# Kernel tuning notes

Measured on AMD Instinct MI355X. Metric: run time of the kernel, lower is better.

## Reference

```python
import jax, jax.numpy as jnp
import numpy as np

T, B, I, H = 512, 32, 512, 512

def setup_inputs() -> dict:
    key = jax.random.key(0)
    k1, k2, k3 = jax.random.split(key, 3)
    x = jax.random.normal(k1, (T, B, I), dtype=jnp.float32)
    h0 = jnp.zeros((B, H), dtype=jnp.float32)
    W_ih = jax.random.normal(k2, (3 * H, I), dtype=jnp.float32) * (1.0 / np.sqrt(H))
    # diagonal recurrent weights, one vector per gate (r, z, n), uniform(-1, 1)
    w_hh = jax.random.uniform(k3, (3, H), dtype=jnp.float32, minval=-1.0, maxval=1.0)
    return {"x": x, "h0": h0, "W_ih": W_ih, "w_hh": w_hh}

def reference(x, h0, W_ih, w_hh):
    # Precompute input-side gate pre-activations for all timesteps: (T, B, 3H)
    gx = jnp.einsum('tbi,gi->tbg', x, W_ih)
    xr, xz, xn = jnp.split(gx, 3, axis=-1)  # each (T, B, H)
    w_r, w_z, w_n = w_hh[0], w_hh[1], w_hh[2]  # each (H,)

    def step(h, g):
        gr, gz, gn = g
        r = jax.nn.sigmoid(gr + w_r * h)
        z = jax.nn.sigmoid(gz + w_z * h)
        n = jnp.tanh(gn + r * (w_n * h))
        h_new = (1.0 - z) * n + z * h
        return h_new, h_new

    h_last, out = jax.lax.scan(step, h0, (xr, xz, xn))
    # out: (T, B, H) all hidden states; h_last: (1, B, H) final state (GRU convention)
    return out, h_last[None, :, :]
```

## Files before the change

kernel.cpp:

```cpp
#include <hip/hip_runtime.h>
#include <hip/hip_bf16.h>
#include <stdint.h>

#define T_DIM 512
#define B_DIM 32
#define K_DIM 512
#define H_DIM 512
#define N_DIM 1536
#define M_DIM 16384

typedef __bf16 bf16_t;
typedef bf16_t bf16x8 __attribute__((ext_vector_type(8)));
typedef float floatx4 __attribute__((ext_vector_type(4)));

#define LOG2E 1.442695041f
#define TWO_LOG2E 2.885390082f

__device__ __forceinline__ unsigned int f2bf_bits(float f) {
  uint32_t u = __builtin_bit_cast(uint32_t, f);
  u += 0x7FFFu + ((u >> 16) & 1u);
  return u >> 16;
}

__global__ void convert_both_kernel(const float* __restrict__ x,
                                    unsigned short* __restrict__ xb,
                                    const float* __restrict__ W,
                                    unsigned short* __restrict__ Wb) {
  int bid = blockIdx.x;
  const float* in;
  unsigned short* out;
  int i;
  if (bid < 4096) {
    in = x; out = xb; i = (bid * 256 + threadIdx.x) * 8;
  } else {
    in = W; out = Wb; i = ((bid - 4096) * 256 + threadIdx.x) * 8;
  }
  const float4* p = (const float4*)(in + i);
  float4 f0 = p[0];
  float4 f1 = p[1];
  uint4 v;
  v.x = f2bf_bits(f0.x) | (f2bf_bits(f0.y) << 16);
  v.y = f2bf_bits(f0.z) | (f2bf_bits(f0.w) << 16);
  v.z = f2bf_bits(f1.x) | (f2bf_bits(f1.y) << 16);
  v.w = f2bf_bits(f1.z) | (f2bf_bits(f1.w) << 16);
  *(uint4*)(out + i) = v;
}

__global__ __launch_bounds__(256) void gemm_bf16_kernel(
    const unsigned short* __restrict__ A, const unsigned short* __restrict__ Bm,
    float* __restrict__ C) {
  __shared__ bf16_t smem[16384];
  const int tid = threadIdx.x;
  const int lane = tid & 63;
  const int w = tid >> 6;
  const int tileM = blockIdx.x * 128;
  const int tileN = blockIdx.y * 128;
  const int waveM = w & 1;
  const int waveN = w >> 1;
  const int lm = lane & 15;
  const int lg = lane >> 4;

  floatx4 acc[4][4] = {};

  for (int k0 = 0; k0 < K_DIM; k0 += 64) {
#pragma unroll
    for (int j = 0; j < 4; ++j) {
      int s = j * 256 + tid;
      int row = s >> 3;
      int cpos = s & 7;
      int kc = cpos ^ (row & 7);
      bf16_t* la = smem + (j * 256 + w * 64) * 8;
      const unsigned short* ga = A + (size_t)(tileM + row) * K_DIM + k0 + kc * 8;
      __builtin_amdgcn_global_load_lds(
          (const __attribute__((address_space(1))) unsigned int*)ga,
          (__attribute__((address_space(3))) unsigned int*)la, 16, 0, 0);
      bf16_t* lb = smem + 8192 + (j * 256 + w * 64) * 8;
      const unsigned short* gb = Bm + (size_t)(tileN + row) * K_DIM + k0 + kc * 8;
      __builtin_amdgcn_global_load_lds(
          (const __attribute__((address_space(1))) unsigned int*)gb,
          (__attribute__((address_space(3))) unsigned int*)lb, 16, 0, 0);
    }
    __syncthreads();

#pragma unroll
    for (int ks = 0; ks < 2; ++ks) {
      bf16x8 af[4], bfg[4];
#pragma unroll
      for (int i = 0; i < 4; ++i) {
        int row = waveM * 64 + i * 16 + lm;
        int c = ks * 4 + lg;
        af[i] = *(const bf16x8*)(smem + row * 64 + (c ^ (row & 7)) * 8);
      }
#pragma unroll
      for (int j = 0; j < 4; ++j) {
        int row = waveN * 64 + j * 16 + lm;
        int c = ks * 4 + lg;
        bfg[j] = *(const bf16x8*)(smem + 8192 + row * 64 + (c ^ (row & 7)) * 8);
      }
#pragma unroll
      for (int i = 0; i < 4; ++i)
#pragma unroll
        for (int j = 0; j < 4; ++j)
          acc[i][j] = __builtin_amdgcn_mfma_f32_16x16x32_bf16(af[i], bfg[j],
                                                              acc[i][j], 0, 0, 0);
    }
    __syncthreads();
  }

  const int row0 = tileM + waveM * 64 + (lane >> 4) * 4;
  const int col0 = tileN + waveN * 64 + lm;
#pragma unroll
  for (int i = 0; i < 4; ++i)
#pragma unroll
    for (int j = 0; j < 4; ++j) {
      const int col = col0 + j * 16;
      const float scl = (col >= 2 * H_DIM) ? TWO_LOG2E : -LOG2E;
#pragma unroll
      for (int r = 0; r < 4; ++r)
        C[(size_t)(row0 + i * 16 + r) * N_DIM + col] = scl * acc[i][j][r];
    }
}

__global__ __launch_bounds__(64) void indgru_scan_kernel(
    const float* __restrict__ gx, const float* __restrict__ h0,
    const float* __restrict__ w_hh, float* __restrict__ out,
    float* __restrict__ hlast) {
  const int idx = blockIdx.x * 64 + threadIdx.x;
  const int b = idx >> 9;
  const int h = idx & (H_DIM - 1);
  const float wr = -LOG2E * w_hh[h];
  const float wz = -LOG2E * w_hh[H_DIM + h];
  const float wn = TWO_LOG2E * w_hh[2 * H_DIM + h];
  float hv = h0[idx];

  const float* base = gx + (size_t)b * N_DIM + H_DIM + h;
  float* outp = out + (size_t)b * H_DIM + h;

  constexpr int D = 16;
  float pr[D], pz[D], pn[D];
#pragma unroll
  for (int t = 0; t < D; ++t) {
    const float* p = base + (size_t)t * (B_DIM * N_DIM);
    pr[t] = p[-H_DIM];
    pz[t] = p[0];
    pn[t] = p[H_DIM];
  }

  for (int t0 = 0; t0 < T_DIM - D; t0 += D) {
#pragma unroll
    for (int s = 0; s < D; ++s) {
      const int t = t0 + s;
      float gr = pr[s], gz = pz[s], gn = pn[s];
      const float* p = base + (size_t)(t + D) * (B_DIM * N_DIM);
      pr[s] = p[-H_DIM];
      pz[s] = p[0];
      pn[s] = p[H_DIM];
      float ar = fmaf(wr, hv, gr);
      float az = fmaf(wz, hv, gz);
      float t1 = wn * hv;
      float er = __builtin_amdgcn_exp2f(ar);
      float ez = __builtin_amdgcn_exp2f(az);
      float r = __builtin_amdgcn_rcpf(1.0f + er);
      float z = __builtin_amdgcn_rcpf(1.0f + ez);
      float en = __builtin_amdgcn_exp2f(fmaf(r, t1, gn));
      float u = __builtin_amdgcn_rcpf(1.0f + en);
      float n = fmaf(-2.0f, u, 1.0f);
      float zh = z * hv;
      float omz = 1.0f - z;
      hv = fmaf(n, omz, zh);
      outp[(size_t)t * (B_DIM * H_DIM)] = hv;
    }
  }
#pragma unroll
  for (int s = 0; s < D; ++s) {
    const int t = T_DIM - D + s;
    float ar = fmaf(wr, hv, pr[s]);
    float az = fmaf(wz, hv, pz[s]);
    float t1 = wn * hv;
    float er = __builtin_amdgcn_exp2f(ar);
    float ez = __builtin_amdgcn_exp2f(az);
    float r = __builtin_amdgcn_rcpf(1.0f + er);
    float z = __builtin_amdgcn_rcpf(1.0f + ez);
    float en = __builtin_amdgcn_exp2f(fmaf(r, t1, pn[s]));
    float u = __builtin_amdgcn_rcpf(1.0f + en);
    float n = fmaf(-2.0f, u, 1.0f);
    float zh = z * hv;
    float omz = 1.0f - z;
    hv = fmaf(n, omz, zh);
    outp[(size_t)t * (B_DIM * H_DIM)] = hv;
  }
  hlast[idx] = hv;
}

extern "C" void kernel_launch(void* const* d_in, const int* in_sizes, int n_in,
                              void* d_out, int out_size, void* d_ws, size_t ws_size,
                              hipStream_t stream) {
  const float* x    = (const float*)d_in[0];
  const float* h0   = (const float*)d_in[1];
  const float* W_ih = (const float*)d_in[2];
  const float* w_hh = (const float*)d_in[3];

  float* out = (float*)d_out;
  float* hlast = out + (size_t)T_DIM * B_DIM * H_DIM;

  char* ws = (char*)d_ws;
  unsigned short* xb = (unsigned short*)ws;
  unsigned short* Wb = (unsigned short*)(ws + 16777216);
  float* gx = (float*)(ws + 16777216 + 1572864);

  convert_both_kernel<<<4480, 256, 0, stream>>>(x, xb, W_ih, Wb);

  dim3 grid(M_DIM / 128, N_DIM / 128);
  gemm_bf16_kernel<<<grid, 256, 0, stream>>>(xb, Wb, gx);

  indgru_scan_kernel<<<256, 64, 0, stream>>>(gx, h0, w_hh, out, hlast);
}
```

Baseline: 172.3 us.

## Interleave gate columns and store GEMM output as fp16 for scan loads

The weight rows are permuted and padded so that the r, z and n gates for each hidden unit sit next to each other, with a zero fourth slot, making N 2048. The GEMM now writes fp16 instead of fp32. The scan then fetches all three gates with one 8-byte load per timestep instead of three scattered fp32 loads, which shrinks the latency-bound loads in the serial recurrence. The cost is a third more GEMM work on the padding columns and reduced precision in the stored pre-activations (fp16 range and rounding).

New measurement: 171.1 us. No clear change (-0.7%).

```diff
diff --git a/kernel.cpp b/kernel.cpp
--- a/kernel.cpp
+++ b/kernel.cpp
@@ -6,7 +6,7 @@
 #define B_DIM 32
 #define K_DIM 512
 #define H_DIM 512
-#define N_DIM 1536
+#define N_PAD 2048
 #define M_DIM 16384
 
 typedef __bf16 bf16_t;
@@ -27,28 +27,42 @@
                                     const float* __restrict__ W,
                                     unsigned short* __restrict__ Wb) {
   int bid = blockIdx.x;
-  const float* in;
-  unsigned short* out;
-  int i;
   if (bid < 4096) {
-    in = x; out = xb; i = (bid * 256 + threadIdx.x) * 8;
+    int i = (bid * 256 + threadIdx.x) * 8;
+    const float4* p = (const float4*)(x + i);
+    float4 f0 = p[0];
+    float4 f1 = p[1];
+    uint4 v;
+    v.x = f2bf_bits(f0.x) | (f2bf_bits(f0.y) << 16);
+    v.y = f2bf_bits(f0.z) | (f2bf_bits(f0.w) << 16);
+    v.z = f2bf_bits(f1.x) | (f2bf_bits(f1.y) << 16);
+    v.w = f2bf_bits(f1.z) | (f2bf_bits(f1.w) << 16);
+    *(uint4*)(xb + i) = v;
   } else {
-    in = W; out = Wb; i = ((bid - 4096) * 256 + threadIdx.x) * 8;
-  }
-  const float4* p = (const float4*)(in + i);
-  float4 f0 = p[0];
-  float4 f1 = p[1];
-  uint4 v;
-  v.x = f2bf_bits(f0.x) | (f2bf_bits(f0.y) << 16);
-  v.y = f2bf_bits(f0.z) | (f2bf_bits(f0.w) << 16);
-  v.z = f2bf_bits(f1.x) | (f2bf_bits(f1.y) << 16);
-  v.w = f2bf_bits(f1.z) | (f2bf_bits(f1.w) << 16);
-  *(uint4*)(out + i) = v;
+    int i = ((bid - 4096) * 256 + threadIdx.x) * 8;
+    int orow = i >> 9;
+    int k = i & 511;
+    int g = orow & 3;
+    int h = orow >> 2;
+    uint4 v;
+    if (g < 3) {
+      const float4* p = (const float4*)(W + ((g << 9) + h) * 512 + k);
+      float4 f0 = p[0];
+      float4 f1 = p[1];
+      v.x = f2bf_bits(f0.x) | (f2bf_bits(f0.y) << 16);
+      v.y = f2bf_bits(f0.z) | (f2bf_bits(f0.w) << 16);
+      v.z = f2bf_bits(f1.x) | (f2bf_bits(f1.y) << 16);
+      v.w = f2bf_bits(f1.z) | (f2bf_bits(f1.w) << 16);
+    } else {
+      v = uint4{0, 0, 0, 0};
+    }
+    *(uint4*)(Wb + i) = v;
+  }
 }
 
 __global__ __launch_bounds__(256) void gemm_bf16_kernel(
     const unsigned short* __restrict__ A, const unsigned short* __restrict__ Bm,
-    float* __restrict__ C) {
+    _Float16* __restrict__ C) {
   __shared__ bf16_t smem[16384];
   const int tid = threadIdx.x;
   const int lane = tid & 63;
@@ -110,19 +124,26 @@
   const int row0 = tileM + waveM * 64 + (lane >> 4) * 4;
   const int col0 = tileN + waveN * 64 + lm;
 #pragma unroll
-  for (int i = 0; i < 4; ++i)
-#pragma unroll
-    for (int j = 0; j < 4; ++j) {
-      const int col = col0 + j * 16;
-      const float scl = (col >= 2 * H_DIM) ? TWO_LOG2E : -LOG2E;
+  for (int j = 0; j < 4; ++j) {
+    const int col = col0 + j * 16;
+    const float scl = ((col & 3) == 2) ? TWO_LOG2E : -LOG2E;
+#pragma unroll
+    for (int i = 0; i < 4; ++i)
 #pragma unroll
       for (int r = 0; r < 4; ++r)
-        C[(size_t)(row0 + i * 16 + r) * N_DIM + col] = scl * acc[i][j][r];
-    }
+        C[(size_t)(row0 + i * 16 + r) * N_PAD + col] = (_Float16)(scl * acc[i][j][r]);
+  }
+}
+
+__device__ __forceinline__ float unpack_lo(uint32_t w16) {
+  return (float)__builtin_bit_cast(_Float16, (unsigned short)(w16 & 0xffff));
+}
+__device__ __forceinline__ float unpack_hi(uint32_t w16) {
+  return (float)__builtin_bit_cast(_Float16, (unsigned short)(w16 >> 16));
 }
 
 __global__ __launch_bounds__(64) void indgru_scan_kernel(
-    const float* __restrict__ gx, const float* __restrict__ h0,
+    const _Float16* __restrict__ gx, const float* __restrict__ h0,
     const float* __restrict__ w_hh, float* __restrict__ out,
     float* __restrict__ hlast) {
   const int idx = blockIdx.x * 64 + threadIdx.x;
@@ -133,28 +154,25 @@
   const float wn = TWO_LOG2E * w_hh[2 * H_DIM + h];
   float hv = h0[idx];
 
-  const float* base = gx + (size_t)b * N_DIM + H_DIM + h;
+  const _Float16* base = gx + ((size_t)b * H_DIM + h) * 4;
   float* outp = out + (size_t)b * H_DIM + h;
 
   constexpr int D = 16;
-  float pr[D], pz[D], pn[D];
-#pragma unroll
-  for (int t = 0; t < D; ++t) {
-    const float* p = base + (size_t)t * (B_DIM * N_DIM);
-    pr[t] = p[-H_DIM];
-    pz[t] = p[0];
-    pn[t] = p[H_DIM];
-  }
+  uint2 pq[D];
+#pragma unroll
+  for (int t = 0; t < D; ++t)
+    pq[t] = *(const uint2*)(base + (size_t)t * (B_DIM * N_PAD));
 
   for (int t0 = 0; t0 < T_DIM - D; t0 += D) {
 #pragma unroll
     for (int s = 0; s < D; ++s) {
       const int t = t0 + s;
-      float gr = pr[s], gz = pz[s], gn = pn[s];
-      const float* p = base + (size_t)(t + D) * (B_DIM * N_DIM);
-      pr[s] = p[-H_DIM];
-      pz[s] = p[0];
-      pn[s] = p[H_DIM];
+      uint2 q = pq[s];
+      pq[s] = *(const uint2*)(base + (size_t)(t + D) * (B_DIM * N_PAD));
+      asm volatile("" ::: "memory");
+      float gr = unpack_lo(q.x);
+      float gz = unpack_hi(q.x);
+      float gn = unpack_lo(q.y);
       float ar = fmaf(wr, hv, gr);
       float az = fmaf(wz, hv, gz);
       float t1 = wn * hv;
@@ -174,14 +192,18 @@
 #pragma unroll
   for (int s = 0; s < D; ++s) {
     const int t = T_DIM - D + s;
-    float ar = fmaf(wr, hv, pr[s]);
-    float az = fmaf(wz, hv, pz[s]);
+    uint2 q = pq[s];
+    float gr = unpack_lo(q.x);
+    float gz = unpack_hi(q.x);
+    float gn = unpack_lo(q.y);
+    float ar = fmaf(wr, hv, gr);
+    float az = fmaf(wz, hv, gz);
     float t1 = wn * hv;
     float er = __builtin_amdgcn_exp2f(ar);
     float ez = __builtin_amdgcn_exp2f(az);
     float r = __builtin_amdgcn_rcpf(1.0f + er);
     float z = __builtin_amdgcn_rcpf(1.0f + ez);
-    float en = __builtin_amdgcn_exp2f(fmaf(r, t1, pn[s]));
+    float en = __builtin_amdgcn_exp2f(fmaf(r, t1, gn));
     float u = __builtin_amdgcn_rcpf(1.0f + en);
     float n = fmaf(-2.0f, u, 1.0f);
     float zh = z * hv;
@@ -206,11 +228,11 @@
   char* ws = (char*)d_ws;
   unsigned short* xb = (unsigned short*)ws;
   unsigned short* Wb = (unsigned short*)(ws + 16777216);
-  float* gx = (float*)(ws + 16777216 + 1572864);
-
-  convert_both_kernel<<<4480, 256, 0, stream>>>(x, xb, W_ih, Wb);
-
-  dim3 grid(M_DIM / 128, N_DIM / 128);
+  _Float16* gx = (_Float16*)(ws + 16777216 + 2097152);
+
+  convert_both_kernel<<<4608, 256, 0, stream>>>(x, xb, W_ih, Wb);
+
+  dim3 grid(M_DIM / 128, N_PAD / 128);
   gemm_bf16_kernel<<<grid, 256, 0, stream>>>(xb, Wb, gx);
 
   indgru_scan_kernel<<<256, 64, 0, stream>>>(gx, h0, w_hh, out, hlast);
```
